# Kernel optimization log

Measured on AMD Instinct MI355X. Metric: run time of the kernel, lower is better.

## Reference

```python
import jax, jax.numpy as jnp
import numpy as np

BATCH, SEQ, HEADS, EMB = 16, 4096, 16, 64
SHAPE = int(SEQ ** 0.5)          # 64 (2D grid side)
N = 2 * SHAPE - 1                # 127 (circular conv length)


def setup_inputs() -> dict:
    key = jax.random.key(0)
    k_v, k_w = jax.random.split(key)
    v = jax.random.normal(k_v, (BATCH, SEQ, HEADS, EMB), dtype=jnp.float32)
    # 'full' bias base: learned relative bias of length 2*shape_-1 per head
    w = jax.random.normal(k_w, (1, HEADS, N), dtype=jnp.float32)
    o_ = jnp.ones((SHAPE,), dtype=jnp.float32)
    return {"v": v, "w": w, "o_": o_}


def reference(v, w, o_):
    B, S, H, E = v.shape
    s = int(S ** 0.5)
    n = 2 * s - 1

    # bias_base_type == 'full': slice w[..., shape_-s : shape_+s-1] == all of w
    z_fft = jnp.fft.rfft(w)                              # (1, H, n//2+1) complex

    # v: [B, S, H, E] -> [B, E, H, s1, s2]
    vt = jnp.transpose(v, (0, 3, 2, 1)).reshape(B, E, H, s, s)
    v_s = vt.sum(axis=3)                                 # sum over s1 -> [B, E, H, s2]
    u_s = vt.sum(axis=4)                                 # sum over s2 -> [B, E, H, s1]

    pad = ((0, 0), (0, 0), (0, 0), (s - 1, 0))
    v_m_fft = jnp.fft.rfft(jnp.pad(v_s, pad))            # [B, E, H, n//2+1]
    u_m_fft = jnp.fft.rfft(jnp.pad(u_s, pad))

    zf = z_fft[:, None]                                  # (1, 1, H, n//2+1)
    RxV = jnp.fft.irfft(v_m_fft * zf, n=n)[..., :s]      # [B, E, H, s]
    RxU = jnp.fft.irfft(u_m_fft * zf, n=n)[..., :s]      # [B, E, H, s]

    # outer sum over the 2D grid, flatten back to seq
    pbv = RxV[..., None, :] + RxU[..., :, None]          # [B, E, H, s, s]
    pbv = pbv.reshape(B, E, H, S)
    pbv = jnp.transpose(pbv, (0, 3, 2, 1))               # [B, S, H, E]

    # normalizer term z_pb (batch independent)
    o_pad = jnp.pad(o_, ((s - 1, 0),))                   # (n,)
    o_fft = jnp.fft.rfft(o_pad)                          # (n//2+1,)
    z_pb = jnp.fft.irfft(o_fft * z_fft, n=n)[..., :s] * s  # (1, H, s)
    z_pb = z_pb[..., None, :] + z_pb[..., :, None]       # (1, H, s, s)
    z_pb = z_pb.reshape(-1, H, s * s)                    # (1, H, S)
    z_pb = jnp.transpose(z_pb, (0, 2, 1))                # (1, S, H)

    return pbv, z_pb
```

## Files before the change

### kernel.cpp

```cpp
#include <hip/hip_runtime.h>

#define BATCH 16
#define SEQ   4096
#define HEADS 16
#define EMB   64
#define SS    64
#define NW    127

__global__ __launch_bounds__(512) void pbv_kernel(const float* __restrict__ v,
                                                  const float* __restrict__ w,
                                                  float* __restrict__ out) {
    __shared__ float us [SS][SS];
    __shared__ float vsf[SS][SS];
    __shared__ float wtab[NW];

    const int bh   = blockIdx.x;
    const int b    = bh / HEADS;
    const int h    = bh % HEADS;
    const int tid  = threadIdx.x;
    const int wave = tid >> 6;
    const int lane = tid & 63;

    for (int idx = tid; idx < SS * SS; idx += 512) (&vsf[0][0])[idx] = 0.0f;
    if (tid < NW) wtab[tid] = w[h * NW + tid];
    __syncthreads();

    const float* vbase = v + ((size_t)b * SEQ * HEADS + h) * EMB + lane;
    float vsacc[SS];
    #pragma unroll
    for (int j = 0; j < SS; ++j) vsacc[j] = 0.0f;

    for (int ii = 0; ii < 8; ++ii) {
        const int i = wave * 8 + ii;
        const float* rowp = vbase + (size_t)i * SS * (HEADS * EMB);
        float uacc = 0.0f;
        #pragma unroll
        for (int j = 0; j < SS; ++j) {
            float val = rowp[(size_t)j * (HEADS * EMB)];
            uacc += val;
            vsacc[j] += val;
        }
        us[i][lane] = uacc;
    }
    #pragma unroll
    for (int j = 0; j < SS; ++j) atomicAdd(&vsf[j][lane], vsacc[j]);
    __syncthreads();

    float rv[8], ru[8];
    for (int tt = 0; tt < 8; ++tt) {
        const int t = wave * 8 + tt;
        float accv = 0.0f, accu = 0.0f;
        #pragma unroll
        for (int j = 0; j < SS; ++j) {
            int k = t - j + 64;
            if (k >= NW) k -= NW;
            const float c = wtab[k];
            accv += c * vsf[j][lane];
            accu += c * us [j][lane];
        }
        rv[tt] = accv;
        ru[tt] = accu;
    }
    __syncthreads();
    for (int tt = 0; tt < 8; ++tt) {
        const int t = wave * 8 + tt;
        vsf[t][lane] = rv[tt];
        us [t][lane] = ru[tt];
    }
    __syncthreads();

    float* obase = out + ((size_t)b * SEQ * HEADS + h) * EMB + lane;
    for (int ii = 0; ii < 8; ++ii) {
        const int i = wave * 8 + ii;
        const float ruv = us[i][lane];
        #pragma unroll
        for (int j = 0; j < SS; ++j) {
            obase[(size_t)(i * SS + j) * (HEADS * EMB)] = vsf[j][lane] + ruv;
        }
    }
}

__global__ __launch_bounds__(256) void zpb_kernel(const float* __restrict__ w,
                                                  const float* __restrict__ o_,
                                                  float* __restrict__ out2) {
    __shared__ float zp[HEADS][SS];
    __shared__ float osh[SS];
    __shared__ float wsh[HEADS * NW];

    const int tid = threadIdx.x;
    const int g   = blockIdx.x;

    if (tid < SS) osh[tid] = o_[tid];
    for (int idx = tid; idx < HEADS * NW; idx += 256) wsh[idx] = w[idx];
    __syncthreads();

    for (int idx = tid; idx < HEADS * SS; idx += 256) {
        const int h = idx / SS, t = idx % SS;
        float acc = 0.0f;
        #pragma unroll
        for (int j = 0; j < SS; ++j) {
            int k = t - j + 64;
            if (k >= NW) k -= NW;
            acc += osh[j] * wsh[h * NW + k];
        }
        zp[h][t] = acc * (float)SS;
    }
    __syncthreads();

    for (int idx = tid; idx < SS * HEADS; idx += 256) {
        const int tl = idx / HEADS, h = idx % HEADS;
        out2[(size_t)(g * SS + tl) * HEADS + h] = zp[h][tl] + zp[h][g];
    }
}

extern "C" void kernel_launch(void* const* d_in, const int* in_sizes, int n_in,
                              void* d_out, int out_size, void* d_ws, size_t ws_size,
                              hipStream_t stream) {
    const float* v  = (const float*)d_in[0];
    const float* w  = (const float*)d_in[1];
    const float* o_ = (const float*)d_in[2];
    float* out = (float*)d_out;

    pbv_kernel<<<BATCH * HEADS, 512, 0, stream>>>(v, w, out);

    const size_t out1_elems = (size_t)BATCH * SEQ * HEADS * EMB;
    zpb_kernel<<<SS, 256, 0, stream>>>(w, o_, out + out1_elems);
}
```

Baseline: 485.4 us.

## Split pbv into row-chunked reduce/conv kernel plus coalesced float4 expand kernel

The single per-(batch,head) kernel is split in two. The first kernel divides each (batch,head) into four row chunks and raises the block count. Each chunk computes partial row sums and the Toeplitz convolutions using register-blocked weights, then accumulates partial RxV/RxU into a zeroed workspace with global atomics. A separate expand kernel writes the outer-sum output with coalesced float4 stores across the full head-by-embedding row. This adds a memset, workspace traffic and global atomics in exchange for more parallelism and better store coalescing.

```diff
diff --git a/kernel.cpp b/kernel.cpp
--- a/kernel.cpp
+++ b/kernel.cpp
@@ -7,21 +7,26 @@
 #define SS    64
 #define NW    127
 
-__global__ __launch_bounds__(512) void pbv_kernel(const float* __restrict__ v,
-                                                  const float* __restrict__ w,
-                                                  float* __restrict__ out) {
-    __shared__ float us [SS][SS];
+#define RX_ELEMS (BATCH * SS * HEADS * EMB)
+
+__global__ __launch_bounds__(256, 4) void reduce_conv_kernel(
+    const float* __restrict__ v, const float* __restrict__ w,
+    float* __restrict__ rxv, float* __restrict__ rxu)
+{
     __shared__ float vsf[SS][SS];
+    __shared__ float usl[16][SS];
     __shared__ float wtab[NW];
 
-    const int bh   = blockIdx.x;
-    const int b    = bh / HEADS;
-    const int h    = bh % HEADS;
+    const int blk  = blockIdx.x;
+    const int c    = blk & 3;
+    const int bh   = blk >> 2;
+    const int b    = bh >> 4;
+    const int h    = bh & (HEADS - 1);
     const int tid  = threadIdx.x;
     const int wave = tid >> 6;
     const int lane = tid & 63;
 
-    for (int idx = tid; idx < SS * SS; idx += 512) (&vsf[0][0])[idx] = 0.0f;
+    for (int idx = tid; idx < SS * SS; idx += 256) (&vsf[0][0])[idx] = 0.0f;
     if (tid < NW) wtab[tid] = w[h * NW + tid];
     __syncthreads();
 
@@ -30,53 +35,90 @@
     #pragma unroll
     for (int j = 0; j < SS; ++j) vsacc[j] = 0.0f;
 
-    for (int ii = 0; ii < 8; ++ii) {
-        const int i = wave * 8 + ii;
+    const int r0 = wave * 4;
+    for (int rr = 0; rr < 4; ++rr) {
+        const int i = c * 16 + r0 + rr;
         const float* rowp = vbase + (size_t)i * SS * (HEADS * EMB);
         float uacc = 0.0f;
         #pragma unroll
         for (int j = 0; j < SS; ++j) {
-            float val = rowp[(size_t)j * (HEADS * EMB)];
+            const float val = rowp[(size_t)j * (HEADS * EMB)];
             uacc += val;
             vsacc[j] += val;
         }
-        us[i][lane] = uacc;
+        usl[r0 + rr][lane] = uacc;
     }
     #pragma unroll
     for (int j = 0; j < SS; ++j) atomicAdd(&vsf[j][lane], vsacc[j]);
     __syncthreads();
 
-    float rv[8], ru[8];
-    for (int tt = 0; tt < 8; ++tt) {
-        const int t = wave * 8 + tt;
-        float accv = 0.0f, accu = 0.0f;
+    const int t0 = wave * 16;
+    float accv[16], accu[16];
+    #pragma unroll
+    for (int tt = 0; tt < 16; ++tt) { accv[tt] = 0.0f; accu[tt] = 0.0f; }
+
+    #pragma unroll
+    for (int jb = 0; jb < 4; ++jb) {
+        float wreg[31];
         #pragma unroll
-        for (int j = 0; j < SS; ++j) {
-            int k = t - j + 64;
-            if (k >= NW) k -= NW;
-            const float c = wtab[k];
-            accv += c * vsf[j][lane];
-            accu += c * us [j][lane];
+        for (int d = 0; d < 31; ++d) {
+            int idx = t0 - jb * 16 + 49 + d;
+            if (idx >= NW) idx -= NW;
+            wreg[d] = wtab[idx];
         }
-        rv[tt] = accv;
-        ru[tt] = accu;
+        #pragma unroll
+        for (int jj = 0; jj < 16; ++jj) {
+            const float cv = vsf[jb * 16 + jj][lane];
+            #pragma unroll
+            for (int tt = 0; tt < 16; ++tt)
+                accv[tt] += wreg[15 + tt - jj] * cv;
+        }
     }
-    __syncthreads();
-    for (int tt = 0; tt < 8; ++tt) {
-        const int t = wave * 8 + tt;
-        vsf[t][lane] = rv[tt];
-        us [t][lane] = ru[tt];
+    {
+        float wreg[31];
+        #pragma unroll
+        for (int d = 0; d < 31; ++d) {
+            int idx = t0 - c * 16 + 49 + d;
+            if (idx >= NW) idx -= NW;
+            wreg[d] = wtab[idx];
+        }
+        #pragma unroll
+        for (int rr = 0; rr < 16; ++rr) {
+            const float cu = usl[rr][lane];
+            #pragma unroll
+            for (int tt = 0; tt < 16; ++tt)
+                accu[tt] += wreg[15 + tt - rr] * cu;
+        }
     }
-    __syncthreads();
 
-    float* obase = out + ((size_t)b * SEQ * HEADS + h) * EMB + lane;
-    for (int ii = 0; ii < 8; ++ii) {
-        const int i = wave * 8 + ii;
-        const float ruv = us[i][lane];
-        #pragma unroll
-        for (int j = 0; j < SS; ++j) {
-            obase[(size_t)(i * SS + j) * (HEADS * EMB)] = vsf[j][lane] + ruv;
-        }
+    const size_t base = (((size_t)b * SS) << 10) + (h << 6) + lane;
+    #pragma unroll
+    for (int tt = 0; tt < 16; ++tt) {
+        const size_t o = base + ((size_t)(t0 + tt) << 10);
+        atomicAdd(&rxv[o], accv[tt]);
+        atomicAdd(&rxu[o], accu[tt]);
+    }
+}
+
+__global__ __launch_bounds__(256) void expand_kernel(
+    const float* __restrict__ rxv, const float* __restrict__ rxu,
+    float* __restrict__ out)
+{
+    const int blk = blockIdx.x;
+    const int b   = blk >> 6;
+    const int tid = threadIdx.x;
+
+    const float4 ru = *((const float4*)(rxu + ((size_t)blk << 10)) + tid);
+    const float4* rvb = (const float4*)(rxv + ((size_t)b << 16));
+    float4* ob = (float4*)(out + (((size_t)blk) << 16)) + tid;
+
+    #pragma unroll 8
+    for (int j = 0; j < SS; ++j) {
+        float4 rv = rvb[(j << 8) + tid];
+        float4 r;
+        r.x = rv.x + ru.x; r.y = rv.y + ru.y;
+        r.z = rv.z + ru.z; r.w = rv.w + ru.w;
+        ob[(size_t)j << 8] = r;
     }
 }
 
@@ -121,7 +163,13 @@
     const float* o_ = (const float*)d_in[2];
     float* out = (float*)d_out;
 
-    pbv_kernel<<<BATCH * HEADS, 512, 0, stream>>>(v, w, out);
+    float* rxv = (float*)d_ws;
+    float* rxu = rxv + RX_ELEMS;
+
+    hipMemsetAsync(d_ws, 0, (size_t)2 * RX_ELEMS * sizeof(float), stream);
+
+    reduce_conv_kernel<<<BATCH * HEADS * 4, 256, 0, stream>>>(v, w, rxv, rxu);
+    expand_kernel<<<BATCH * SS, 256, 0, stream>>>(rxv, rxu, out);
 
     const size_t out1_elems = (size_t)BATCH * SEQ * HEADS * EMB;
     zpb_kernel<<<SS, 256, 0, stream>>>(w, o_, out + out1_elems);
```

After: 567.2 us. +16.9%, slower.

## Split row/column sums into separate float4-vectorized kernel with workspace partials

Applied to the files above, without the earlier changes.

Replaces the fused per-(batch,head) kernel with two kernels. The first reads v with float4 loads, with each block covering a quarter of the sequence and all heads for a channel slice, and writes partial column sums and row sums to workspace. The second kernel reduces the partials and runs the Toeplitz convolution with register-blocked weights, then writes the expanded output. This aims to make the 268MB input read coalesced and better parallelized, at the cost of an extra launch and workspace traffic. The old path is kept as a fallback when the workspace is too small.

```diff
diff --git a/kernel.cpp b/kernel.cpp
--- a/kernel.cpp
+++ b/kernel.cpp
@@ -6,6 +6,145 @@
 #define EMB   64
 #define SS    64
 #define NW    127
+#define PLANE (HEADS * EMB)
+
+#define US_ELEMS    (BATCH * SS * PLANE)
+#define VPART_ELEMS (BATCH * 4 * SS * PLANE)
+#define WS_NEEDED ((size_t)(VPART_ELEMS + US_ELEMS) * sizeof(float))
+
+__global__ __launch_bounds__(256) void sums_kernel(
+    const float4* __restrict__ v4, float4* __restrict__ vpart4,
+    float4* __restrict__ us4)
+{
+    __shared__ float4 u_lds[4][16][64];
+
+    const int blk = blockIdx.x;
+    const int b   = blk >> 4;
+    const int q   = (blk >> 2) & 3;
+    const int cq  = blk & 3;
+    const int tid = threadIdx.x;
+    const int w   = tid >> 6;
+    const int c4  = tid & 63;
+
+    const float4* base = v4 + (((size_t)(b * SEQ + q * 1024)) << 8)
+                            + (cq << 6) + c4;
+
+    float4 vacc[16];
+    #pragma unroll
+    for (int m = 0; m < 16; ++m) vacc[m] = make_float4(0.f, 0.f, 0.f, 0.f);
+
+    for (int il = 0; il < 16; ++il) {
+        float4 uacc = make_float4(0.f, 0.f, 0.f, 0.f);
+        #pragma unroll
+        for (int m = 0; m < 16; ++m) {
+            const float4 x = base[(size_t)((il << 6) + w + (m << 2)) << 8];
+            uacc.x += x.x; uacc.y += x.y; uacc.z += x.z; uacc.w += x.w;
+            vacc[m].x += x.x; vacc[m].y += x.y;
+            vacc[m].z += x.z; vacc[m].w += x.w;
+        }
+        u_lds[w][il][c4] = uacc;
+    }
+    __syncthreads();
+
+    {
+        int s = tid;
+        #pragma unroll
+        for (int r = 0; r < 4; ++r, s += 256) {
+            const int il = s >> 6, c = s & 63;
+            float4 a = u_lds[0][il][c];
+            #pragma unroll
+            for (int ww = 1; ww < 4; ++ww) {
+                const float4 x = u_lds[ww][il][c];
+                a.x += x.x; a.y += x.y; a.z += x.z; a.w += x.w;
+            }
+            us4[((size_t)((b << 6) + (q << 4) + il) << 8) + (cq << 6) + c] = a;
+        }
+    }
+
+    #pragma unroll
+    for (int m = 0; m < 16; ++m) {
+        const int j = w + (m << 2);
+        vpart4[((size_t)((((b << 2) + q) << 6) + j) << 8) + (cq << 6) + c4]
+            = vacc[m];
+    }
+}
+
+__global__ __launch_bounds__(512) void convexp_kernel(
+    const float* __restrict__ w, const float4* __restrict__ vpart4,
+    const float4* __restrict__ us4, float* __restrict__ out)
+{
+    __shared__ float wtab[NW];
+    __shared__ float vsl[SS][SS];
+    __shared__ float usl[SS][SS];
+
+    const int bh   = blockIdx.x;
+    const int b    = bh >> 4;
+    const int h    = bh & (HEADS - 1);
+    const int tid  = threadIdx.x;
+    const int wave = tid >> 6;
+    const int lane = tid & 63;
+
+    if (tid < NW) wtab[tid] = w[h * NW + tid];
+
+    for (int s = tid; s < SS * 16; s += 512) {
+        const int j = s >> 4, e4 = s & 15;
+        float4 acc = make_float4(0.f, 0.f, 0.f, 0.f);
+        #pragma unroll
+        for (int q = 0; q < 4; ++q) {
+            const float4 x =
+                vpart4[((size_t)((((b << 2) + q) << 6) + j) << 8) + (h << 4) + e4];
+            acc.x += x.x; acc.y += x.y; acc.z += x.z; acc.w += x.w;
+        }
+        *(float4*)&vsl[j][e4 << 2] = acc;
+        *(float4*)&usl[j][e4 << 2] =
+            us4[((size_t)((b << 6) + j) << 8) + (h << 4) + e4];
+    }
+    __syncthreads();
+
+    const int t0 = wave << 3;
+    float accv[8], accu[8];
+    #pragma unroll
+    for (int tt = 0; tt < 8; ++tt) { accv[tt] = 0.0f; accu[tt] = 0.0f; }
+
+    #pragma unroll
+    for (int jb = 0; jb < 4; ++jb) {
+        float wreg[23];
+        #pragma unroll
+        for (int d = 0; d < 23; ++d) {
+            int idx = t0 - (jb << 4) + 49 + d;
+            if (idx >= NW) idx -= NW;
+            wreg[d] = wtab[idx];
+        }
+        #pragma unroll
+        for (int jj = 0; jj < 16; ++jj) {
+            const float cv = vsl[(jb << 4) + jj][lane];
+            const float cu = usl[(jb << 4) + jj][lane];
+            #pragma unroll
+            for (int tt = 0; tt < 8; ++tt) {
+                const float cw = wreg[15 + tt - jj];
+                accv[tt] += cw * cv;
+                accu[tt] += cw * cu;
+            }
+        }
+    }
+    __syncthreads();
+    #pragma unroll
+    for (int tt = 0; tt < 8; ++tt) {
+        vsl[t0 + tt][lane] = accv[tt];
+        usl[t0 + tt][lane] = accu[tt];
+    }
+    __syncthreads();
+
+    float* obase = out + (((size_t)b * SEQ) << 10) + (h << 6) + lane;
+    for (int ii = 0; ii < 8; ++ii) {
+        const int i = (wave << 3) + ii;
+        const float ruv = usl[i][lane];
+        #pragma unroll
+        for (int j = 0; j < SS; ++j) {
+            obase[(size_t)((i << 6) + j) << 10] = vsl[j][lane] + ruv;
+        }
+    }
+}
 
 __global__ __launch_bounds__(512) void pbv_kernel(const float* __restrict__ v,
                                                   const float* __restrict__ w,
@@ -121,7 +260,17 @@
     const float* o_ = (const float*)d_in[2];
     float* out = (float*)d_out;
 
-    pbv_kernel<<<BATCH * HEADS, 512, 0, stream>>>(v, w, out);
+    if (ws_size >= WS_NEEDED) {
+        float* vpart = (float*)d_ws;
+        float* us    = vpart + VPART_ELEMS;
+
+        sums_kernel<<<256, 256, 0, stream>>>(
+            (const float4*)v, (float4*)vpart, (float4*)us);
+        convexp_kernel<<<BATCH * HEADS, 512, 0, stream>>>(
+            w, (const float4*)vpart, (const float4*)us, out);
+    } else {
+        pbv_kernel<<<BATCH * HEADS, 512, 0, stream>>>(v, w, out);
+    }
 
     const size_t out1_elems = (size_t)BATCH * SEQ * HEADS * EMB;
     zpb_kernel<<<SS, 256, 0, stream>>>(w, o_, out + out1_elems);
```

Result: faster. 461.4 us (-4.9%).
